# Performance work log

Hardware: AMD Instinct MI355X
Metric: run time of the kernel (lower is better)

Reference implementation:

```python
import jax, jax.numpy as jnp
import numpy as np

N = 50000          # neuron_count
NNZ = 1_600_000    # edges (avg degree 32)
B = 32             # batch
L = 3              # CONNECTOME_LAYER_NUMBER


def setup_inputs() -> dict:
    key = jax.random.key(0)
    k1, k2, k3, k4, k5 = jax.random.split(key, 5)
    x = jax.random.normal(k1, (B, N), dtype=jnp.float32)
    adj_vals = jax.random.uniform(k2, (NNZ,), dtype=jnp.float32)
    w_vals = jax.random.uniform(k3, (NNZ,), dtype=jnp.float32)
    bias = jnp.ones((N,), dtype=jnp.float32)
    row = jax.random.randint(k4, (NNZ,), 0, N, dtype=jnp.int32)
    col = jax.random.randint(k5, (NNZ,), 0, N, dtype=jnp.int32)
    return {"x": x, "adj_vals": adj_vals, "w_vals": w_vals, "bias": bias,
            "row": row, "col": col}


def _spmm(vals, row, col, dense, n):
    # (sparse NxN) @ dense [N, B] via gather + segment_sum scatter
    contrib = vals[:, None] * dense[col]          # [nnz, B]
    return jax.ops.segment_sum(contrib, row, num_segments=n)


def reference(x, adj_vals, w_vals, bias, row, col):
    # Original per layer: x = ((A @ W) @ x^T)^T + bias.
    # We use associativity: (A @ W) @ x^T == A @ (W @ x^T), avoiding the
    # explicit SpGEMM while computing the same linear map.
    n = bias.shape[0]
    xt = x.T                                      # [N, B]
    for _ in range(L):
        wx = _spmm(w_vals, row, col, xt, n)       # W @ x^T -> [N, B]
        xt = _spmm(adj_vals, row, col, wx, n)     # A @ (W @ x^T)
        xt = xt + bias[:, None]                   # broadcast bias over batch
    return xt.T                                   # [B, N]
```

## Files before the change

### kernel.cpp

```cpp
#include <hip/hip_runtime.h>


#define NN 50000
#define NNZ_E 1600000
#define NB (NN * 32)
#define CHUNK 6144
#define NBLK1 ((NNZ_E + CHUNK - 1) / CHUNK)
#define NBIN ((NN + 127) / 128)
#define NH (NBIN * NBLK1)
#define CAP2 5120
#define BCAP 6144
#define LENP (NBIN * BCAP)
#define SCAN_NBLK ((NH + 255) / 256)

__device__ __forceinline__ int clampi(int v, int hi) {
    v = v < 0 ? 0 : v;
    return v > hi ? hi : v;
}

__device__ __forceinline__ unsigned short f2h(float v) {
    union { _Float16 h; unsigned short u; } cv;
    cv.h = (_Float16)v;
    return cv.u;
}

__device__ __forceinline__ _Float16 kv_val_h(unsigned kv) {
    union { unsigned short u; _Float16 h; } cv;
    cv.u = (unsigned short)(kv >> 16);
    return cv.h;
}

__global__ __launch_bounds__(256) void hist_kernel(const int* __restrict__ row,
                                                   int* __restrict__ hist1) {
    __shared__ int h[NBIN];
    int blk = blockIdx.x, tid = threadIdx.x;
    for (int j = tid; j < NBIN; j += 256) h[j] = 0;
    __syncthreads();
    int base = blk * CHUNK;
    int n = NNZ_E - base; if (n > CHUNK) n = CHUNK;
    for (int i = tid; i < n; i += 256)
        atomicAdd(&h[clampi(row[base + i], NN - 1) >> 7], 1);
    __syncthreads();
    for (int j = tid; j < NBIN; j += 256) hist1[j * NBLK1 + blk] = h[j];
}

__global__ void scan_local_kernel(int* __restrict__ data, int n, int* __restrict__ bsum) {
    __shared__ int s[256];
    int i = blockIdx.x * 256 + threadIdx.x;
    int v = (i < n) ? data[i] : 0;
    s[threadIdx.x] = v;
    __syncthreads();
    for (int off = 1; off < 256; off <<= 1) {
        int t = (threadIdx.x >= off) ? s[threadIdx.x - off] : 0;
        __syncthreads();
        s[threadIdx.x] += t;
        __syncthreads();
    }
    if (i < n) data[i] = s[threadIdx.x] - v;
    if (threadIdx.x == 255) bsum[blockIdx.x] = s[threadIdx.x];
}

__global__ void scan_tops_kernel(int* __restrict__ bsum, int m) {
    __shared__ int s[512];
    int t = threadIdx.x;
    int v = (t < m) ? bsum[t] : 0;
    s[t] = v;
    __syncthreads();
    for (int off = 1; off < 512; off <<= 1) {
        int u = (t >= off) ? s[t - off] : 0;
        __syncthreads();
        s[t] += u;
        __syncthreads();
    }
    if (t < m) bsum[t] = s[t] - v;
}

__global__ void fin_add_kernel(int* __restrict__ data, int n, const int* __restrict__ bsum) {
    int i = blockIdx.x * blockDim.x + threadIdx.x;
    if (i < n) data[i] += bsum[i >> 8];
}

__global__ void binstart_kernel(const int* __restrict__ hist1, int* __restrict__ binstart) {
    int j = blockIdx.x * blockDim.x + threadIdx.x;
    if (j < NBIN) binstart[j] = hist1[j * NBLK1];
    if (j == 0) binstart[NBIN] = NNZ_E;
}

__global__ __launch_bounds__(256) void pass1_kernel(
        const int* __restrict__ row, const int* __restrict__ col,
        const float* __restrict__ a, const float* __restrict__ w,
        const int* __restrict__ hist1_off,
        unsigned* __restrict__ k1, unsigned* __restrict__ aw1) {
    __shared__ int h[NBIN];
    __shared__ int hscan[NBIN];
    __shared__ int hoff[NBIN];
    __shared__ int s256[256];
    __shared__ unsigned sKey[CHUNK];
    __shared__ unsigned sAW[CHUNK];
    int blk = blockIdx.x, tid = threadIdx.x;
    int base = blk * CHUNK;
    int n = NNZ_E - base; if (n > CHUNK) n = CHUNK;

    for (int j = tid; j < NBIN; j += 256) {
        h[j] = 0;
        hoff[j] = hist1_off[j * NBLK1 + blk];
    }
    __syncthreads();
    for (int i = tid; i < n; i += 256)
        atomicAdd(&h[clampi(row[base + i], NN - 1) >> 7], 1);
    __syncthreads();
    int j0 = tid * 2, j1 = tid * 2 + 1;
    int c0 = (j0 < NBIN) ? h[j0] : 0;
    int c1 = (j1 < NBIN) ? h[j1] : 0;
    int tsum = c0 + c1;
    s256[tid] = tsum;
    __syncthreads();
    for (int off = 1; off < 256; off <<= 1) {
        int t = (tid >= off) ? s256[tid - off] : 0;
        __syncthreads();
        s256[tid] += t;
        __syncthreads();
    }
    int ex = s256[tid] - tsum;
    __syncthreads();
    if (j0 < NBIN) { hscan[j0] = ex;      h[j0] = ex; }
    if (j1 < NBIN) { hscan[j1] = ex + c0; h[j1] = ex + c0; }
    __syncthreads();
    for (int i = tid; i < n; i += 256) {
        int r = clampi(row[base + i], NN - 1);
        int c = clampi(col[base + i], NN - 1);
        int bin = r >> 7;
        int p = atomicAdd(&h[bin], 1);
        p = clampi(p, n - 1);
        sKey[p] = ((unsigned)r << 16) | (unsigned)c;
        sAW[p] = ((unsigned)f2h(a[base + i]) << 16) | (unsigned)f2h(w[base + i]);
    }
    __syncthreads();
    for (int p = tid; p < n; p += 256) {
        unsigned key = sKey[p];
        int bin = (int)(key >> 23);
        int d = clampi(hoff[bin] + (p - hscan[bin]), NNZ_E - 1);
        k1[d] = key;
        aw1[d] = sAW[p];
    }
}

__global__ __launch_bounds__(256) void pass2_kernel(
        const unsigned* __restrict__ k1, const unsigned* __restrict__ aw1,
        const int* __restrict__ binstart,
        unsigned* __restrict__ kvA2, unsigned* __restrict__ kvW2,
        unsigned* __restrict__ sdesc, int* __restrict__ srow) {
    __shared__ unsigned sKey[CAP2];
    __shared__ unsigned sAW[CAP2];
    __shared__ int rh[128];
    __shared__ int rs[128];
    __shared__ int cur[128];
    __shared__ int rofsS[128];
    __shared__ int cnt64[64];
    int bin = blockIdx.x, tid = threadIdx.x;
    int r0 = bin << 7;
    int rows = NN - r0; if (rows > 128) rows = 128;
    int base = clampi(binstart[bin], NNZ_E);
    int size = clampi(binstart[bin + 1], NNZ_E) - base;
    size = clampi(size, CAP2);
    int pbase = bin * BCAP;

    if (tid < 128) rh[tid] = 0;
    if (tid < 64) cnt64[tid] = 0;
    __syncthreads();
    for (int i = tid; i < size; i += 256) {
        unsigned key = k1[base + i];
        atomicAdd(&rh[(key >> 16) & 127], 1);
        sKey[i] = key;
        sAW[i] = aw1[base + i];
    }
    __syncthreads();
    int cnt  = (tid < 128) ? rh[tid] : 0;
    int plen = (cnt + 7) & ~7;
    if (tid < 128) rs[tid] = plen;
    __syncthreads();
    for (int off = 1; off < 128; off <<= 1) {
        int t = (tid >= off && tid < 128) ? rs[tid - off] : 0;
        __syncthreads();
        if (tid < 128) rs[tid] += t;
        __syncthreads();
    }
    int rofs = (tid < 128) ? clampi(rs[tid] - plen, BCAP - 8) : 0;
    if (tid < 128) { cur[tid] = rofs; rofsS[tid] = rofs; }
    int niter = plen >> 3;
    int skey = clampi(niter, 63);
    if (tid < rows) atomicAdd(&cnt64[skey], 1);
    __syncthreads();
    if (tid == 0) {
        int acc = 0;
        for (int q = 0; q < 64; ++q) { int v = cnt64[q]; cnt64[q] = acc; acc += v; }
    }
    __syncthreads();
    if (tid < rows) {
        int si = atomicAdd(&cnt64[skey], 1);
        si = clampi(si, rows - 1);
        sdesc[r0 + si] = (unsigned)(pbase + rofs) | ((unsigned)niter << 24);
        srow[r0 + si]  = r0 + tid;
    }
    __syncthreads();
    for (int i = tid; i < size; i += 256) {
        unsigned key = sKey[i];
        unsigned aw  = sAW[i];
        int rl = (key >> 16) & 127;
        int p = atomicAdd(&cur[rl], 1);
        p = clampi(p, BCAP - 1);
        unsigned c = key & 0xFFFFu;
        kvA2[pbase + p] = (aw & 0xFFFF0000u) | c;
        kvW2[pbase + p] = (aw << 16) | c;
    }
    __syncthreads();
    if (tid < rows) {
        int pl = (rh[tid] + 7) & ~7;
        for (int q = rh[tid]; q < pl; ++q) {
            int d = clampi(rofsS[tid] + q, BCAP - 1);
            kvA2[pbase + d] = 0u;
            kvW2[pbase + d] = 0u;
        }
    }
}

__global__ void transpose_in_kernel(const float* __restrict__ x,
                                    _Float16* __restrict__ xt) {
    int i = blockIdx.x * blockDim.x + threadIdx.x;
    if (i < NB) {
        int n = i >> 5;
        int b = i & 31;
        xt[i] = (_Float16)x[b * NN + n];
    }
}

template <int WITH_BIAS>
__global__ __launch_bounds__(256) void spmm_kernel(
        const uint2* __restrict__ kv2, const unsigned* __restrict__ sdesc,
        const int* __restrict__ srow,
        const uint2* __restrict__ in64, uint2* __restrict__ out64,
        const float* __restrict__ bias, float outScale, float biasScale) {
    int t = blockIdx.x * 256 + threadIdx.x;
    int g = t >> 3;
    int l = t & 7;
    if (g >= NN) return;
    unsigned d = sdesc[g];
    int r = clampi(srow[g], NN - 1);
    int niter = (int)(d >> 24);
    int base2 = clampi((int)(d & 0xFFFFFFu), LENP - 8) >> 1;
    float a0 = 0.0f, a1 = 0.0f, a2 = 0.0f, a3 = 0.0f;
    uint2 k2[4];
    if (niter > 0) {
#pragma unroll
        for (int q = 0; q < 4; ++q) k2[q] = kv2[base2 + q];
    }
    for (int it = 0; it < niter; ++it) {
        unsigned k[8];
#pragma unroll
        for (int q = 0; q < 4; ++q) { k[2 * q] = k2[q].x; k[2 * q + 1] = k2[q].y; }
        uint2 gd[8];
#pragma unroll
        for (int j = 0; j < 8; ++j) gd[j] = in64[((k[j] & 0xFFFFu) << 3) + l];
        if (it + 1 < niter) {
            int nb2 = base2 + (it + 1) * 4;
#pragma unroll
            for (int q = 0; q < 4; ++q) k2[q] = kv2[nb2 + q];
        }
#pragma unroll
        for (int j = 0; j < 8; ++j) {
            _Float16 vh = kv_val_h(k[j]);
            union { uint2 u; _Float16 h[4]; } cv;
            cv.u = gd[j];
            a0 += (float)vh * (float)cv.h[0];
            a1 += (float)vh * (float)cv.h[1];
            a2 += (float)vh * (float)cv.h[2];
            a3 += (float)vh * (float)cv.h[3];
        }
    }
    float r0 = a0 * outScale, r1 = a1 * outScale;
    float r2 = a2 * outScale, r3 = a3 * outScale;
    if (WITH_BIAS) {
        float bb = bias[r] * biasScale;
        r0 += bb; r1 += bb; r2 += bb; r3 += bb;
    }
    union { uint2 u; _Float16 h[4]; } o;
    o.h[0] = (_Float16)r0; o.h[1] = (_Float16)r1;
    o.h[2] = (_Float16)r2; o.h[3] = (_Float16)r3;
    out64[(r << 3) + l] = o.u;
}

__global__ void transpose_out_kernel(const _Float16* __restrict__ xt,
                                     float* __restrict__ out) {
    int i = blockIdx.x * blockDim.x + threadIdx.x;
    if (i < NB) {
        int b = i / NN;
        int n = i - b * NN;
        out[i] = (float)xt[(n << 5) + b] * 16777216.0f;
    }
}

extern "C" void kernel_launch(void* const* d_in, const int* in_sizes, int n_in,
                              void* d_out, int out_size, void* d_ws, size_t ws_size,
                              hipStream_t stream) {
    const float* x        = (const float*)d_in[0];
    const float* adj_vals = (const float*)d_in[1];
    const float* w_vals   = (const float*)d_in[2];
    const float* bias     = (const float*)d_in[3];
    const int*   row      = (const int*)d_in[4];
    const int*   col      = (const int*)d_in[5];
    float* out = (float*)d_out;

    unsigned*  k1        = (unsigned*)d_ws;
    unsigned*  aw1       = k1 + NNZ_E;
    unsigned*  kvA2      = aw1 + NNZ_E;
    unsigned*  kvW2      = kvA2 + LENP;
    _Float16*  xt16      = (_Float16*)(kvW2 + LENP);
    _Float16*  tmp16     = xt16 + NB;
    int*   hist1         = (int*)(tmp16 + NB);
    int*   bsumB         = hist1 + NH;
    int*   binstart      = bsumB + 512;
    unsigned* sdesc      = (unsigned*)(binstart + NBIN + 8);
    int*      srow       = (int*)(sdesc + NN + 8);

    const int BS = 256;
    const int grid_nb   = (NB + BS - 1) / BS;
    const int grid_spmm = (NN * 8 + BS - 1) / BS;

    hist_kernel<<<NBLK1, BS, 0, stream>>>(row, hist1);
    scan_local_kernel<<<SCAN_NBLK, BS, 0, stream>>>(hist1, NH, bsumB);
    scan_tops_kernel<<<1, 512, 0, stream>>>(bsumB, SCAN_NBLK);
    fin_add_kernel<<<SCAN_NBLK, BS, 0, stream>>>(hist1, NH, bsumB);
    binstart_kernel<<<(NBIN + 1 + BS - 1) / BS, BS, 0, stream>>>(hist1, binstart);

    pass1_kernel<<<NBLK1, BS, 0, stream>>>(row, col, adj_vals, w_vals,
                                           hist1, k1, aw1);
    pass2_kernel<<<NBIN, BS, 0, stream>>>(k1, aw1, binstart, kvA2, kvW2,
                                          sdesc, srow);

    const uint2* kvA = (const uint2*)kvA2;
    const uint2* kvW = (const uint2*)kvW2;
    const uint2* xtg  = (const uint2*)xt16;
    uint2*       xtgw = (uint2*)xt16;
    const uint2* tmg  = (const uint2*)tmp16;
    uint2*       tmgw = (uint2*)tmp16;

    transpose_in_kernel<<<grid_nb, BS, 0, stream>>>(x, xt16);
    const float r256 = 1.0f / 256.0f;
    float biasScale = 1.0f;
    for (int layer = 0; layer < 3; ++layer) {
        biasScale *= r256;
        spmm_kernel<0><<<grid_spmm, BS, 0, stream>>>(kvW, sdesc, srow, xtg, tmgw,
                                                     nullptr, 1.0f, 0.0f);
        spmm_kernel<1><<<grid_spmm, BS, 0, stream>>>(kvA, sdesc, srow, tmg, xtgw,
                                                     bias, r256, biasScale);
    }
    transpose_out_kernel<<<grid_nb, BS, 0, stream>>>(xt16, out);
}
```

Baseline: 261.5 us.

## Use 16 lanes per row in SpMM and prefetch next gather batch

Each output row now gets 16 threads, each handling 2 fp16 batch columns through 32-bit loads, instead of 8 threads handling 4 columns through 64-bit loads. The main loop also software-pipelines the dense gathers: the next iteration's key/value words and gathered inputs are loaded before the current batch is accumulated. This aims for more memory-level parallelism and shorter dependency chains per thread. The cost is twice as many threads, each re-reading the same kv descriptors, narrower loads, and more registers for the double-buffered state.

Measured after the change: 263.3 us. No clear change (+0.7%).

```diff
diff --git a/kernel.cpp b/kernel.cpp
--- a/kernel.cpp
+++ b/kernel.cpp
@@ -24,10 +24,10 @@
     return cv.u;
 }
 
-__device__ __forceinline__ _Float16 kv_val_h(unsigned kv) {
+__device__ __forceinline__ float kv_val(unsigned kv) {
     union { unsigned short u; _Float16 h; } cv;
     cv.u = (unsigned short)(kv >> 16);
-    return cv.h;
+    return (float)cv.h;
 }
 
 __global__ __launch_bounds__(256) void hist_kernel(const int* __restrict__ row,
@@ -238,55 +238,65 @@
 __global__ __launch_bounds__(256) void spmm_kernel(
         const uint2* __restrict__ kv2, const unsigned* __restrict__ sdesc,
         const int* __restrict__ srow,
-        const uint2* __restrict__ in64, uint2* __restrict__ out64,
+        const unsigned* __restrict__ in32, unsigned* __restrict__ out32,
         const float* __restrict__ bias, float outScale, float biasScale) {
     int t = blockIdx.x * 256 + threadIdx.x;
-    int g = t >> 3;
-    int l = t & 7;
+    int g = t >> 4;
+    int l = t & 15;
     if (g >= NN) return;
     unsigned d = sdesc[g];
     int r = clampi(srow[g], NN - 1);
     int niter = (int)(d >> 24);
     int base2 = clampi((int)(d & 0xFFFFFFu), LENP - 8) >> 1;
-    float a0 = 0.0f, a1 = 0.0f, a2 = 0.0f, a3 = 0.0f;
-    uint2 k2[4];
+    float accL = 0.0f, accH = 0.0f;
+    uint2 k2[4], k2n[4];
+    unsigned gd[8], gdn[8];
     if (niter > 0) {
 #pragma unroll
         for (int q = 0; q < 4; ++q) k2[q] = kv2[base2 + q];
+#pragma unroll
+        for (int q = 0; q < 4; ++q) {
+            gd[2 * q]     = in32[((k2[q].x & 0xFFFFu) << 4) + l];
+            gd[2 * q + 1] = in32[((k2[q].y & 0xFFFFu) << 4) + l];
+        }
     }
     for (int it = 0; it < niter; ++it) {
-        unsigned k[8];
-#pragma unroll
-        for (int q = 0; q < 4; ++q) { k[2 * q] = k2[q].x; k[2 * q + 1] = k2[q].y; }
-        uint2 gd[8];
-#pragma unroll
-        for (int j = 0; j < 8; ++j) gd[j] = in64[((k[j] & 0xFFFFu) << 3) + l];
         if (it + 1 < niter) {
             int nb2 = base2 + (it + 1) * 4;
 #pragma unroll
-            for (int q = 0; q < 4; ++q) k2[q] = kv2[nb2 + q];
+            for (int q = 0; q < 4; ++q) k2n[q] = kv2[nb2 + q];
+#pragma unroll
+            for (int q = 0; q < 4; ++q) {
+                gdn[2 * q]     = in32[((k2n[q].x & 0xFFFFu) << 4) + l];
+                gdn[2 * q + 1] = in32[((k2n[q].y & 0xFFFFu) << 4) + l];
+            }
         }
 #pragma unroll
-        for (int j = 0; j < 8; ++j) {
-            _Float16 vh = kv_val_h(k[j]);
-            union { uint2 u; _Float16 h[4]; } cv;
-            cv.u = gd[j];
-            a0 += (float)vh * (float)cv.h[0];
-            a1 += (float)vh * (float)cv.h[1];
-            a2 += (float)vh * (float)cv.h[2];
-            a3 += (float)vh * (float)cv.h[3];
+        for (int q = 0; q < 4; ++q) {
+            float vx = kv_val(k2[q].x);
+            float vy = kv_val(k2[q].y);
+            union { unsigned u; _Float16 h[2]; } cx, cy;
+            cx.u = gd[2 * q];
+            cy.u = gd[2 * q + 1];
+            accL += vx * (float)cx.h[0];
+            accH += vx * (float)cx.h[1];
+            accL += vy * (float)cy.h[0];
+            accH += vy * (float)cy.h[1];
         }
-    }
-    float r0 = a0 * outScale, r1 = a1 * outScale;
-    float r2 = a2 * outScale, r3 = a3 * outScale;
+#pragma unroll
+        for (int q = 0; q < 4; ++q) k2[q] = k2n[q];
+#pragma unroll
+        for (int j = 0; j < 8; ++j) gd[j] = gdn[j];
+    }
+    float rL = accL * outScale, rH = accH * outScale;
     if (WITH_BIAS) {
         float bb = bias[r] * biasScale;
-        r0 += bb; r1 += bb; r2 += bb; r3 += bb;
-    }
-    union { uint2 u; _Float16 h[4]; } o;
-    o.h[0] = (_Float16)r0; o.h[1] = (_Float16)r1;
-    o.h[2] = (_Float16)r2; o.h[3] = (_Float16)r3;
-    out64[(r << 3) + l] = o.u;
+        rL += bb; rH += bb;
+    }
+    union { unsigned u; _Float16 h[2]; } o;
+    o.h[0] = (_Float16)rL;
+    o.h[1] = (_Float16)rH;
+    out32[(r << 4) + l] = o.u;
 }
 
 __global__ void transpose_out_kernel(const _Float16* __restrict__ xt,
@@ -324,7 +334,7 @@
 
     const int BS = 256;
     const int grid_nb   = (NB + BS - 1) / BS;
-    const int grid_spmm = (NN * 8 + BS - 1) / BS;
+    const int grid_spmm = (NN * 16 + BS - 1) / BS;
 
     hist_kernel<<<NBLK1, BS, 0, stream>>>(row, hist1);
     scan_local_kernel<<<SCAN_NBLK, BS, 0, stream>>>(hist1, NH, bsumB);
@@ -339,19 +349,19 @@
 
     const uint2* kvA = (const uint2*)kvA2;
     const uint2* kvW = (const uint2*)kvW2;
-    const uint2* xtg  = (const uint2*)xt16;
-    uint2*       xtgw = (uint2*)xt16;
-    const uint2* tmg  = (const uint2*)tmp16;
-    uint2*       tmgw = (uint2*)tmp16;
+    const unsigned* xt32  = (const unsigned*)xt16;
+    unsigned*       xt32w = (unsigned*)xt16;
+    const unsigned* tm32  = (const unsigned*)tmp16;
+    unsigned*       tm32w = (unsigned*)tmp16;
 
     transpose_in_kernel<<<grid_nb, BS, 0, stream>>>(x, xt16);
     const float r256 = 1.0f / 256.0f;
     float biasScale = 1.0f;
     for (int layer = 0; layer < 3; ++layer) {
         biasScale *= r256;
-        spmm_kernel<0><<<grid_spmm, BS, 0, stream>>>(kvW, sdesc, srow, xtg, tmgw,
+        spmm_kernel<0><<<grid_spmm, BS, 0, stream>>>(kvW, sdesc, srow, xt32, tm32w,
                                                      nullptr, 1.0f, 0.0f);
-        spmm_kernel<1><<<grid_spmm, BS, 0, stream>>>(kvA, sdesc, srow, tmg, xtgw,
+        spmm_kernel<1><<<grid_spmm, BS, 0, stream>>>(kvA, sdesc, srow, tm32, xt32w,
                                                      bias, r256, biasScale);
     }
     transpose_out_kernel<<<grid_nb, BS, 0, stream>>>(xt16, out);
```
